# Optimization experiments

Hardware: AMD Instinct MI355X
Metric: run time of the kernel (lower is better)

The kernel has to match this reference:

```python
import jax, jax.numpy as jnp
import numpy as np

IN_DIM = 64
OUT_DIM = 128
GROUPS = 4
KS = 3
PAD = 1
SPLINE_ORDER = 3
GRID_SIZE = 5
GRID_K = GRID_SIZE + SPLINE_ORDER  # 8
GRID_LO, GRID_HI = -1.0, 1.0
_H = (GRID_HI - GRID_LO) / GRID_SIZE
GRID = jnp.linspace(GRID_LO - _H * SPLINE_ORDER, GRID_HI + _H * SPLINE_ORDER,
                    GRID_SIZE + 2 * SPLINE_ORDER + 1, dtype=jnp.float32)  # [14]
EPS = 1e-5


def _conv(x, w):
    # NCHW x OIHW -> NCHW, stride 1, dilation 1, padding PAD
    return jax.lax.conv_general_dilated(
        x, w, window_strides=(1, 1), padding=((PAD, PAD), (PAD, PAD)),
        dimension_numbers=('NCHW', 'OIHW', 'NCHW'))


def _bspline_bases(x):
    # Cox-de-Boor recursion; x: [B,C,H,W] -> [B, C*GRID_K, H, W]
    xu = x[..., None]  # [B,C,H,W,1]
    g = GRID
    bases = ((xu >= g[:-1]) & (xu < g[1:])).astype(x.dtype)  # [B,C,H,W,13]
    for k in range(1, SPLINE_ORDER + 1):
        left = g[:-(k + 1)]
        right = g[k:-1]
        delta = jnp.where(right == left, jnp.ones_like(right), right - left)
        bases = ((xu - left) / delta * bases[..., :-1]
                 + (g[k + 1:] - xu) / (g[k + 1:] - g[1:-k]) * bases[..., 1:])
    B, C, H, W, K = bases.shape  # K == GRID_K
    # moveaxis(-1, 2) then flatten(1, 2): channel-major, basis-minor ordering
    return jnp.moveaxis(bases, -1, 2).reshape(B, C * K, H, W)


def setup_inputs() -> dict:
    key = jax.random.key(0)
    k1, k2 = jax.random.split(key)
    x = jax.random.normal(k1, (8, IN_DIM, 64, 64), dtype=jnp.float32)
    # layer_weight: [out/g, (in/g)*(grid_k+1), ks, ks] = [32, 144, 3, 3]
    layer_weight = jax.random.normal(
        k2, (OUT_DIM // GROUPS, (IN_DIM // GROUPS) * (GRID_K + 1), KS, KS),
        dtype=jnp.float32) * 0.05
    prelu_w = jnp.full((GROUPS,), 0.25, dtype=jnp.float32)  # torch PReLU init
    return {"x": x, "layer_weight": layer_weight, "prelu_w": prelu_w}


def reference(x, layer_weight, prelu_w):
    cin_g = IN_DIM // GROUPS
    cout_g = OUT_DIM // GROUPS
    base_w = layer_weight[:, -cin_g:].reshape(cout_g, cin_g, KS, KS)
    spline_w = layer_weight[:, :-cin_g].reshape(cout_g, cin_g * GRID_K, KS, KS)
    outs = []
    for g in range(GROUPS):
        xg = x[:, g * cin_g:(g + 1) * cin_g]
        base_out = _conv(jax.nn.gelu(xg, approximate=False), base_w)
        spline_out = _conv(_bspline_bases(xg), spline_w)
        y = base_out + spline_out
        # InstanceNorm2d (affine=False): per-sample per-channel spatial norm
        mu = y.mean(axis=(2, 3), keepdims=True)
        var = y.var(axis=(2, 3), keepdims=True)
        y = (y - mu) / jnp.sqrt(var + EPS)
        # PReLU with scalar slope per group
        y = jnp.where(y >= 0, y, prelu_w[g] * y)
        outs.append(y)
    return jnp.concatenate(outs, axis=1)  # [B, OUT_DIM, H, W]
```

## Files before the change

### kernel.cpp

```cpp
#include <hip/hip_runtime.h>
#include <hip/hip_bf16.h>
#include <math.h>

typedef __attribute__((ext_vector_type(8))) short short8;
typedef __attribute__((ext_vector_type(4))) float f32x4;
typedef __attribute__((ext_vector_type(16))) float f32x16;
typedef unsigned int u32;
typedef unsigned long long u64;

__device__ __forceinline__ ushort f2bf(float f) {
    u32 u = __float_as_uint(f);
    return (ushort)((u + 0x7fffu + ((u >> 16) & 1u)) >> 16);
}
__device__ __forceinline__ float bf2f(ushort h) {
    return __uint_as_float(((u32)h) << 16);
}
__device__ __forceinline__ u32 cvtpk_bf16(float a, float b) {
    u32 r;
    asm("v_cvt_pk_bf16_f32 %0, %1, %2" : "=v"(r) : "v"(a), "v"(b));
    return r;
}

#define RS 144

__global__ void wtrans(const float* __restrict__ lw, ushort* __restrict__ w2) {
    int t = blockIdx.x * 256 + threadIdx.x;
    if (t >= 5184) return;
    int l    = t & 63;
    int page = t >> 6;
    int ks  = page % 9;
    int tap = page / 9;
    int oc = l & 31;
    int kbase = ks * 16 + ((l >> 5) << 3);
    short8 v;
#pragma unroll
    for (int e = 0; e < 8; ++e) {
        int k = kbase + e;
        v[e] = (short)f2bf(lw[(oc * 144 + k) * 9 + tap]);
    }
    ((short8*)w2)[t] = v;
}

__global__ __launch_bounds__(256, 5) void kanconv(const float* __restrict__ x,
                                                  const ushort* __restrict__ w2,
                                                  ushort* __restrict__ yraw) {
    __shared__ __align__(16) ushort Fs[109 * RS];
    const int tid  = threadIdx.x;
    const int bx   = blockIdx.x;
    const int tile = ((bx & 7) << 3) | (bx >> 3);
    const int b    = blockIdx.y;
    const int g    = blockIdx.z;
    const int h0 = (tile >> 2) * 4;
    const int w0 = (tile & 3) * 16;
    const float* xg = x + ((size_t)(b * 64 + g * 16)) * 4096;

    float xv1[4], xv2[4];
    unsigned imgbits = 0;
#pragma unroll
    for (int it = 0; it < 4; ++it) {
        int e = it * 256 + tid;
        int icg = e / 108;
        int p   = e - icg * 108;
        int py = p / 18, px = p - py * 18;
        int hy = h0 + py - 1, wx = w0 + px - 1;
        bool valid = (e < 864) && ((unsigned)hy < 64u) && ((unsigned)wx < 64u);
        int off = valid ? (icg * 4096 + hy * 64 + wx) : 0;
        float a = xg[off];
        float c = xg[off + 8 * 4096];
        if (!valid) { a = 0.f; c = 0.f; } else { imgbits |= (1u << it); }
        xv1[it] = a;
        xv2[it] = c;
    }

#define STAGE(V, IMGF, ROWP, SLOT)                                            \
    do {                                                                      \
        float v_ = (V);                                                       \
        float tpos_ = (v_ + 2.2f) * 2.5f;                                     \
        float cf_ = floorf(tpos_);                                            \
        int ci_ = (int)cf_;                                                   \
        float u_ = tpos_ - cf_;                                               \
        float u2_ = u_ * u_, u3_ = u2_ * u_, om_ = 1.f - u_;                  \
        float q0_ = om_ * om_ * om_ * (1.f / 6.f);                            \
        float q1_ = (4.f - 6.f * u2_ + 3.f * u3_) * (1.f / 6.f);              \
        float q2_ = (1.f + 3.f * u_ + 3.f * u2_ - 3.f * u3_) * (1.f / 6.f);   \
        float q3_ = u3_ * (1.f / 6.f);                                        \
        u64 Q_ = (u64)cvtpk_bf16(q0_, q1_)                                    \
               | ((u64)cvtpk_bf16(q2_, q3_) << 32);                           \
        u64 lo_ = 0, hi_ = 0;                                                 \
        if ((IMGF) && ci_ >= 0 && ci_ <= 10) {                                \
            int s_ = ci_ * 16 - 48;                                           \
            if (s_ < 0)       { lo_ = Q_ >> (-s_); }                          \
            else if (s_ < 64) { lo_ = Q_ << s_;                               \
                                hi_ = s_ ? (Q_ >> (64 - s_)) : 0ull; }        \
            else              { hi_ = Q_ << (s_ - 64); }                      \
        }                                                                     \
        union { u64 q[2]; short8 s8; } un_;                                   \
        un_.q[0] = lo_; un_.q[1] = hi_;                                       \
        ushort* row_ = &Fs[(ROWP) * RS];                                      \
        *(short8*)(row_ + (SLOT) * 8) = un_.s8;                               \
        float x3_ = v_ * v_ * v_;                                             \
        float t2_ = fmaf(0.0713548163f, x3_, 1.5957691216f * v_);             \
        float e2_ = __expf(t2_);                                              \
        float th_ = 1.f - 2.f / (e2_ + 1.f);                                  \
        float ge_ = 0.5f * v_ * (1.f + th_);                                  \
        row_[128 + (SLOT)] = f2bf(ge_);                                       \
    } while (0)

#define STAGE_IT(IT, XV, SB)                                                  \
    do {                                                                      \
        int e_ = (IT) * 256 + tid;                                            \
        int icg_ = e_ / 108;                                                  \
        int p_ = e_ - icg_ * 108;                                             \
        int rowp_ = (e_ < 864) ? p_ : 108;         \
        bool im_ = (imgbits >> (IT)) & 1u;                                    \
        STAGE((XV)[IT], im_, rowp_, icg_ + (SB));                             \
    } while (0)

    STAGE_IT(0, xv1, 0);
    STAGE_IT(1, xv1, 0);
    STAGE_IT(2, xv1, 0);
    STAGE_IT(3, xv1, 0);
    __syncthreads();

    const int wv = tid >> 6;
    const int l  = tid & 63;
    const int la = l & 31, klo = l >> 5;
    const int p0row = la >> 4, p0col = la & 15;
    const short8* w8 = (const short8*)w2;

    f32x16 accA, accB;
#pragma unroll
    for (int i = 0; i < 16; ++i) { accA[i] = 0.f; accB[i] = 0.f; }

#define TAPKS(TAP, K0, K1)                                                     \
    do {                                                                       \
        const int kh_ = (TAP) / 3, kw_ = (TAP) - kh_ * 3;                      \
        const ushort* fb0_ =                                                   \
            &Fs[((p0row + kh_) * 18 + (p0col + kw_)) * RS + klo * 8];          \
        const ushort* fb1_ = fb0_ + 2 * 18 * RS;                               \
        const short8* ap_ = w8 + (TAP) * 576 + l;                              \
        _Pragma("unroll")                                                      \
        for (int ks_ = (K0); ks_ < (K1); ++ks_) {                              \
            short8 a_  = ap_[ks_ * 64];                                        \
            short8 b0_ = *(const short8*)(fb0_ + ks_ * 16);                    \
            short8 b1_ = *(const short8*)(fb1_ + ks_ * 16);                    \
            accA = __builtin_amdgcn_mfma_f32_32x32x16_bf16(a_, b0_, accA, 0, 0, 0); \
            accB = __builtin_amdgcn_mfma_f32_32x32x16_bf16(a_, b1_, accB, 0, 0, 0); \
        }                                                                      \
    } while (0)

    const int t0 = wv * 2, t1 = wv * 2 + 1;

    STAGE_IT(0, xv2, 8);
    STAGE_IT(1, xv2, 8);
    TAPKS(t0, 0, 2);
    STAGE_IT(2, xv2, 8);
    TAPKS(t0, 2, 4);
    STAGE_IT(3, xv2, 8);
    TAPKS(t1, 0, 4);
    if (wv == 3) TAPKS(8, 0, 4);
    __syncthreads();

    TAPKS(t0, 4, 9);
    TAPKS(t1, 4, 9);
    if (wv == 3) TAPKS(8, 4, 9);
#undef TAPKS
#undef STAGE_IT
#undef STAGE

    __syncthreads();
    float* comb = (float*)Fs;
    if (wv != 0) {
        float* cp = comb + ((wv - 1) * 64 + l) * 20;
        *(f32x4*)(cp + 0)  = f32x4{accA[0], accA[1], accA[2], accA[3]};
        *(f32x4*)(cp + 4)  = f32x4{accA[4], accA[5], accA[6], accA[7]};
        *(f32x4*)(cp + 8)  = f32x4{accA[8], accA[9], accA[10], accA[11]};
        *(f32x4*)(cp + 12) = f32x4{accA[12], accA[13], accA[14], accA[15]};
    }
    if (wv != 1) {
        int slot = (wv == 0) ? 3 : (2 + wv);
        float* cp = comb + (slot * 64 + l) * 20;
        *(f32x4*)(cp + 0)  = f32x4{accB[0], accB[1], accB[2], accB[3]};
        *(f32x4*)(cp + 4)  = f32x4{accB[4], accB[5], accB[6], accB[7]};
        *(f32x4*)(cp + 8)  = f32x4{accB[8], accB[9], accB[10], accB[11]};
        *(f32x4*)(cp + 12) = f32x4{accB[12], accB[13], accB[14], accB[15]};
    }
    __syncthreads();
    if (wv < 2) {
        f32x16 sum = (wv == 0) ? accA : accB;
        const int sbase = (wv == 0) ? 0 : 3;
#pragma unroll
        for (int s = 0; s < 3; ++s) {
            const float* cp = comb + ((sbase + s) * 64 + l) * 20;
            f32x4 c0 = *(const f32x4*)(cp + 0);
            f32x4 c1 = *(const f32x4*)(cp + 4);
            f32x4 c2 = *(const f32x4*)(cp + 8);
            f32x4 c3 = *(const f32x4*)(cp + 12);
#pragma unroll
            for (int r = 0; r < 4; ++r) {
                sum[r]      += c0[r];
                sum[r + 4]  += c1[r];
                sum[r + 8]  += c2[r];
                sum[r + 12] += c3[r];
            }
        }
        const int pix = wv * 32 + la;
        const int prow = pix >> 4, pcol = pix & 15;
        ushort* yb = yraw + (((size_t)b * 128 + g * 32) * 64 + h0 + prow) * 64
                          + w0 + pcol;
#pragma unroll
        for (int r = 0; r < 16; ++r) {
            int oc = (r & 3) + 8 * (r >> 2) + 4 * klo;
            yb[(size_t)oc * 4096] = f2bf(sum[r]);
        }
    }
}

__global__ __launch_bounds__(512) void instnorm(const ushort* __restrict__ yraw,
                                                float* __restrict__ y,
                                                const float* __restrict__ prelu) {
    const int blk = blockIdx.x;
    const int tid = threadIdx.x;
    const short8* rp = (const short8*)(yraw + (size_t)blk * 4096);
    short8 a = rp[tid];
    float v[8];
#pragma unroll
    for (int j = 0; j < 8; ++j) v[j] = bf2f((ushort)a[j]);
    float s = 0.f, s2 = 0.f;
#pragma unroll
    for (int j = 0; j < 8; ++j) { s += v[j]; s2 += v[j] * v[j]; }
#pragma unroll
    for (int off = 32; off > 0; off >>= 1) {
        s  += __shfl_down(s, off);
        s2 += __shfl_down(s2, off);
    }
    __shared__ float red[16];
    int wave = tid >> 6;
    if ((tid & 63) == 0) { red[wave] = s; red[8 + wave] = s2; }
    __syncthreads();
    float S  = red[0] + red[1] + red[2] + red[3]
             + red[4] + red[5] + red[6] + red[7];
    float S2 = red[8] + red[9] + red[10] + red[11]
             + red[12] + red[13] + red[14] + red[15];
    float mean = S * (1.0f / 4096.0f);
    float var  = S2 * (1.0f / 4096.0f) - mean * mean;
    float rstd = rsqrtf(var + 1e-5f);
    float slope = prelu[(blk >> 5) & 3];
    float4* op = (float4*)(y + (size_t)blk * 4096) + tid * 2;
#pragma unroll
    for (int k = 0; k < 2; ++k) {
        float4 o;
        float t;
        t = (v[k * 4 + 0] - mean) * rstd; o.x = t >= 0.f ? t : slope * t;
        t = (v[k * 4 + 1] - mean) * rstd; o.y = t >= 0.f ? t : slope * t;
        t = (v[k * 4 + 2] - mean) * rstd; o.z = t >= 0.f ? t : slope * t;
        t = (v[k * 4 + 3] - mean) * rstd; o.w = t >= 0.f ? t : slope * t;
        op[k] = o;
    }
}

extern "C" void kernel_launch(void* const* d_in, const int* in_sizes, int n_in,
                              void* d_out, int out_size, void* d_ws, size_t ws_size,
                              hipStream_t stream) {
    const float* x     = (const float*)d_in[0];
    const float* lw    = (const float*)d_in[1];
    const float* prelu = (const float*)d_in[2];
    float*  out  = (float*)d_out;
    ushort* w2   = (ushort*)d_ws;
    ushort* yraw = (ushort*)((char*)d_ws + 92160);

    wtrans<<<21, 256, 0, stream>>>(lw, w2);
    dim3 grid(64, 8, 4);
    kanconv<<<grid, 256, 0, stream>>>(x, w2, yraw);
    instnorm<<<1024, 512, 0, stream>>>(yraw, out, prelu);
}
```

Baseline: 37.17 us.

## Fuse instance-norm statistics into conv epilogue via atomics

```diff
diff --git a/kernel.cpp b/kernel.cpp
--- a/kernel.cpp
+++ b/kernel.cpp
@@ -23,7 +23,12 @@
 
 #define RS 144
 
-__global__ void wtrans(const float* __restrict__ lw, ushort* __restrict__ w2) {
+__global__ void wtrans(const float* __restrict__ lw, ushort* __restrict__ w2,
+                       float* __restrict__ st) {
+    if (blockIdx.x == 21) {
+        for (int i = threadIdx.x; i < 2048; i += 256) st[i] = 0.f;
+        return;
+    }
     int t = blockIdx.x * 256 + threadIdx.x;
     if (t >= 5184) return;
     int l    = t & 63;
@@ -43,7 +48,8 @@
 
 __global__ __launch_bounds__(256, 5) void kanconv(const float* __restrict__ x,
                                                   const ushort* __restrict__ w2,
-                                                  ushort* __restrict__ yraw) {
+                                                  ushort* __restrict__ yraw,
+                                                  float* __restrict__ st) {
     __shared__ __align__(16) ushort Fs[109 * RS];
     const int tid  = threadIdx.x;
     const int bx   = blockIdx.x;
@@ -213,50 +219,53 @@
             int oc = (r & 3) + 8 * (r >> 2) + 4 * klo;
             yb[(size_t)oc * 4096] = f2bf(sum[r]);
         }
-    }
-}
-
-__global__ __launch_bounds__(512) void instnorm(const ushort* __restrict__ yraw,
+        float s_[16], q_[16];
+#pragma unroll
+        for (int r = 0; r < 16; ++r) { s_[r] = sum[r]; q_[r] = sum[r] * sum[r]; }
+#pragma unroll
+        for (int off = 16; off >= 1; off >>= 1) {
+#pragma unroll
+            for (int r = 0; r < 16; ++r) {
+                s_[r] += __shfl_xor(s_[r], off);
+                q_[r] += __shfl_xor(q_[r], off);
+            }
+        }
+        if (la == 0) {
+#pragma unroll
+            for (int r = 0; r < 16; ++r) {
+                int oc = (r & 3) + 8 * (r >> 2) + 4 * klo;
+                float* sp = st + (((size_t)b * 128 + g * 32 + oc) << 1);
+                atomicAdd(sp,     s_[r]);
+                atomicAdd(sp + 1, q_[r]);
+            }
+        }
+    }
+}
+
+__global__ __launch_bounds__(256) void instnorm(const ushort* __restrict__ yraw,
+                                                const float* __restrict__ st,
                                                 float* __restrict__ y,
                                                 const float* __restrict__ prelu) {
-    const int blk = blockIdx.x;
-    const int tid = threadIdx.x;
-    const short8* rp = (const short8*)(yraw + (size_t)blk * 4096);
-    short8 a = rp[tid];
-    float v[8];
-#pragma unroll
-    for (int j = 0; j < 8; ++j) v[j] = bf2f((ushort)a[j]);
-    float s = 0.f, s2 = 0.f;
-#pragma unroll
-    for (int j = 0; j < 8; ++j) { s += v[j]; s2 += v[j] * v[j]; }
-#pragma unroll
-    for (int off = 32; off > 0; off >>= 1) {
-        s  += __shfl_down(s, off);
-        s2 += __shfl_down(s2, off);
-    }
-    __shared__ float red[16];
-    int wave = tid >> 6;
-    if ((tid & 63) == 0) { red[wave] = s; red[8 + wave] = s2; }
-    __syncthreads();
-    float S  = red[0] + red[1] + red[2] + red[3]
-             + red[4] + red[5] + red[6] + red[7];
-    float S2 = red[8] + red[9] + red[10] + red[11]
-             + red[12] + red[13] + red[14] + red[15];
-    float mean = S * (1.0f / 4096.0f);
-    float var  = S2 * (1.0f / 4096.0f) - mean * mean;
-    float rstd = rsqrtf(var + 1e-5f);
+    const int t = blockIdx.x * 256 + threadIdx.x;
+    const int blk = t >> 9;
+    float mean = st[blk * 2]     * (1.0f / 4096.0f);
+    float ex2  = st[blk * 2 + 1] * (1.0f / 4096.0f);
+    float rstd = rsqrtf(ex2 - mean * mean + 1e-5f);
     float slope = prelu[(blk >> 5) & 3];
-    float4* op = (float4*)(y + (size_t)blk * 4096) + tid * 2;
-#pragma unroll
-    for (int k = 0; k < 2; ++k) {
-        float4 o;
-        float t;
-        t = (v[k * 4 + 0] - mean) * rstd; o.x = t >= 0.f ? t : slope * t;
-        t = (v[k * 4 + 1] - mean) * rstd; o.y = t >= 0.f ? t : slope * t;
-        t = (v[k * 4 + 2] - mean) * rstd; o.z = t >= 0.f ? t : slope * t;
-        t = (v[k * 4 + 3] - mean) * rstd; o.w = t >= 0.f ? t : slope * t;
-        op[k] = o;
-    }
+    short8 a = *(const short8*)(yraw + (size_t)t * 8);
+    float4* op = (float4*)(y + (size_t)t * 8);
+    float4 o0, o1;
+    float v;
+    v = (bf2f((ushort)a[0]) - mean) * rstd; o0.x = v >= 0.f ? v : slope * v;
+    v = (bf2f((ushort)a[1]) - mean) * rstd; o0.y = v >= 0.f ? v : slope * v;
+    v = (bf2f((ushort)a[2]) - mean) * rstd; o0.z = v >= 0.f ? v : slope * v;
+    v = (bf2f((ushort)a[3]) - mean) * rstd; o0.w = v >= 0.f ? v : slope * v;
+    v = (bf2f((ushort)a[4]) - mean) * rstd; o1.x = v >= 0.f ? v : slope * v;
+    v = (bf2f((ushort)a[5]) - mean) * rstd; o1.y = v >= 0.f ? v : slope * v;
+    v = (bf2f((ushort)a[6]) - mean) * rstd; o1.z = v >= 0.f ? v : slope * v;
+    v = (bf2f((ushort)a[7]) - mean) * rstd; o1.w = v >= 0.f ? v : slope * v;
+    op[0] = o0;
+    op[1] = o1;
 }
 
 extern "C" void kernel_launch(void* const* d_in, const int* in_sizes, int n_in,
@@ -268,9 +277,10 @@
     float*  out  = (float*)d_out;
     ushort* w2   = (ushort*)d_ws;
     ushort* yraw = (ushort*)((char*)d_ws + 92160);
-
-    wtrans<<<21, 256, 0, stream>>>(lw, w2);
+    float*  st   = (float*)((char*)d_ws + 92160 + 8388608);
+
+    wtrans<<<22, 256, 0, stream>>>(lw, w2, st);
     dim3 grid(64, 8, 4);
-    kanconv<<<grid, 256, 0, stream>>>(x, w2, yraw);
-    instnorm<<<1024, 512, 0, stream>>>(yraw, out, prelu);
-}
+    kanconv<<<grid, 256, 0, stream>>>(x, w2, yraw, st);
+    instnorm<<<2048, 256, 0, stream>>>(yraw, st, out, prelu);
+}
```

After: 85.98 us. +131.3%, slower.
